# Kernel optimization log

Hardware: AMD Instinct MI355X
Metric: run time of the kernel (lower is better)

The kernel has to match this reference:

```python
import jax, jax.numpy as jnp
import numpy as np

NUM_GRAPHS = 128

def setup_inputs() -> dict:
    key = jax.random.key(0)
    ks = jax.random.split(key, 12)
    N, E = 50000, 800000
    x = jax.random.normal(ks[0], (N, 54), dtype=jnp.float32)
    edge_index = jax.random.randint(ks[1], (2, E), 0, N, dtype=jnp.int64)
    batch = jnp.sort(jax.random.randint(ks[2], (N,), 0, NUM_GRAPHS, dtype=jnp.int64))
    def lin(k, fi, fo):
        return jax.random.normal(k, (fi, fo), dtype=jnp.float32) / np.sqrt(fi)
    return {
        "x": x, "edge_index": edge_index, "batch": batch,
        "W1l": lin(ks[3], 54, 128), "b1": jnp.zeros((128,), jnp.float32), "W1r": lin(ks[4], 54, 128),
        "W2l": lin(ks[5], 128, 256), "b2": jnp.zeros((256,), jnp.float32), "W2r": lin(ks[6], 128, 256),
        "W3l": lin(ks[7], 256, 256), "b3": jnp.zeros((256,), jnp.float32), "W3r": lin(ks[8], 256, 256),
    }

def _sage(h, src, dst, n, Wl, b, Wr):
    # sum-aggregate neighbor features x_j (j=src) into node i (i=dst), then
    # out = lin_l(agg) + lin_r(h)  (PyG SAGEConv, aggr='sum')
    agg = jax.ops.segment_sum(h[src], dst, num_segments=n)
    return jax.nn.relu(agg @ Wl + b + h @ Wr)

def reference(x, edge_index, batch, W1l, b1, W1r, W2l, b2, W2r, W3l, b3, W3r):
    n = x.shape[0]
    src, dst = edge_index[0], edge_index[1]
    h = _sage(x, src, dst, n, W1l, b1, W1r)
    h = _sage(h, src, dst, n, W2l, b2, W2r)
    h = _sage(h, src, dst, n, W3l, b3, W3r)
    # global mean pool per graph (gep = global_mean_pool)
    sums = jax.ops.segment_sum(h, batch, num_segments=NUM_GRAPHS)
    cnts = jax.ops.segment_sum(jnp.ones((n, 1), h.dtype), batch, num_segments=NUM_GRAPHS)
    return sums / jnp.maximum(cnts, 1.0)
```

## Files before the change

### kernel.cpp

```cpp
#include <hip/hip_runtime.h>


typedef unsigned short u16;
typedef __attribute__((ext_vector_type(8))) short bf16x8;
typedef __attribute__((ext_vector_type(4))) float f32x4;

__device__ __forceinline__ u16 f2b(float f) {
    union { float f; unsigned u; } v; v.f = f;
    unsigned u = v.u;
    return (u16)((u + 0x7FFF + ((u >> 16) & 1)) >> 16);
}
__device__ __forceinline__ float b2f(u16 h) {
    union { unsigned u; float f; } v; v.u = ((unsigned)h) << 16;
    return v.f;
}
__device__ __forceinline__ float blo(unsigned u) {
    union { unsigned u; float f; } v; v.u = u << 16;
    return v.f;
}
__device__ __forceinline__ float bhi(unsigned u) {
    union { unsigned u; float f; } v; v.u = u & 0xffff0000u;
    return v.f;
}

__global__ void k_prep(const float* __restrict__ x,
                       const float* __restrict__ W1l, const float* __restrict__ W1r,
                       const float* __restrict__ W2l, const float* __restrict__ W2r,
                       const float* __restrict__ W3l, const float* __restrict__ W3r,
                       u16* __restrict__ xb,
                       u16* __restrict__ wt1l, u16* __restrict__ wt1r,
                       u16* __restrict__ wt2l, u16* __restrict__ wt2r,
                       u16* __restrict__ wt3l, u16* __restrict__ wt3r, int N) {
    long idx = (long)blockIdx.x * 256 + threadIdx.x;
    long s0 = (long)N * 54;
    if (idx < s0) { xb[idx] = f2b(x[idx]); return; }
    idx -= s0;
    if (idx < 2 * 128 * 64) {
        u16* o = (idx < 128 * 64) ? wt1l : wt1r;
        const float* w = (idx < 128 * 64) ? W1l : W1r;
        long loc = idx % (128 * 64);
        int d = (int)(loc >> 6), k = (int)(loc & 63);
        o[loc] = (k < 54) ? f2b(w[(long)k * 128 + d]) : 0;
        return;
    }
    idx -= 2 * 128 * 64;
    if (idx < 2 * 256 * 128) {
        u16* o = (idx < 256 * 128) ? wt2l : wt2r;
        const float* w = (idx < 256 * 128) ? W2l : W2r;
        long loc = idx % (256 * 128);
        int d = (int)(loc >> 7), k = (int)(loc & 127);
        o[loc] = f2b(w[(long)k * 256 + d]);
        return;
    }
    idx -= 2 * 256 * 128;
    if (idx < 2 * 256 * 256) {
        u16* o = (idx < 256 * 256) ? wt3l : wt3r;
        const float* w = (idx < 256 * 256) ? W3l : W3r;
        long loc = idx % (256 * 256);
        int d = (int)(loc >> 8), k = (int)(loc & 255);
        o[loc] = f2b(w[(long)k * 256 + d]);
    }
}

__global__ void k_count(const int* __restrict__ dst, int* __restrict__ cnt, int E) {
    int e = blockIdx.x * 256 + threadIdx.x;
    if (e < E) atomicAdd(&cnt[dst[e]], 1);
}

__global__ void k_bsum(const int* __restrict__ cnt, int* __restrict__ bsum, int N) {
    __shared__ int sm[256];
    int i = blockIdx.x * 256 + threadIdx.x;
    sm[threadIdx.x] = (i < N) ? cnt[i] : 0;
    __syncthreads();
    for (int off = 128; off > 0; off >>= 1) {
        if (threadIdx.x < off) sm[threadIdx.x] += sm[threadIdx.x + off];
        __syncthreads();
    }
    if (threadIdx.x == 0) bsum[blockIdx.x] = sm[0];
}

__global__ void k_bscan(const int* __restrict__ bsum, int* __restrict__ boff, int NB) {
    __shared__ int sm[256];
    int t = threadIdx.x;
    int v = (t < NB) ? bsum[t] : 0;
    sm[t] = v;
    __syncthreads();
    for (int off = 1; off < 256; off <<= 1) {
        int add = (t >= off) ? sm[t - off] : 0;
        __syncthreads();
        sm[t] += add;
        __syncthreads();
    }
    if (t < NB) boff[t] = sm[t] - v;
}

__global__ void k_scan(const int* __restrict__ cnt, const int* __restrict__ boff,
                       int* __restrict__ rowptr, int* __restrict__ wpos, int N, int E) {
    __shared__ int sm[256];
    int t = threadIdx.x;
    int i = blockIdx.x * 256 + t;
    int v = (i < N) ? cnt[i] : 0;
    sm[t] = v;
    __syncthreads();
    for (int off = 1; off < 256; off <<= 1) {
        int add = (t >= off) ? sm[t - off] : 0;
        __syncthreads();
        sm[t] += add;
        __syncthreads();
    }
    int ex = sm[t] - v + boff[blockIdx.x];
    if (i < N) { rowptr[i] = ex; wpos[i] = ex; }
    if (i == 0) rowptr[N] = E;
}

__global__ void k_fill(const int* __restrict__ src, const int* __restrict__ dst,
                       int* __restrict__ wpos, int* __restrict__ csr, int E) {
    int e = blockIdx.x * 256 + threadIdx.x;
    if (e < E) {
        int p = atomicAdd(&wpos[dst[e]], 1);
        csr[p] = src[e];
    }
}

template <int KA, int KW, int DOUT, int EPW>
__global__ __launch_bounds__(512) void k_fused(const u16* __restrict__ h,
                                               const int* __restrict__ rowptr,
                                               const int* __restrict__ csr,
                                               const u16* __restrict__ Wt1,
                                               const u16* __restrict__ Wt2,
                                               const float* __restrict__ bias,
                                               u16* __restrict__ C, int N) {
    constexpr int KAP = KW + 8;
    constexpr int WCOL = DOUT / 4;
    constexpr int FN = WCOL / 16;
    __shared__ u16 aggL[64 * KAP];
    __shared__ u16 xL[(KA == 54) ? 64 * KAP : 8];
    __shared__ u16 Bs[DOUT * 40];

    const int tid = threadIdx.x;
    const int w = tid >> 6, lane = tid & 63;
    const int m0 = blockIdx.x * 64;

    for (int t = 0; t < 8; ++t) {
        int r = w * 8 + t;
        int node = m0 + r;
        if constexpr (KA == 54) {
            u16 xv = 0;
            if (node < N && lane < 54) xv = h[(size_t)node * 54 + lane];
            xL[r * KAP + lane] = xv;
            float a = 0.f;
            if (node < N && lane < 54) {
                int b0 = rowptr[node], b1 = rowptr[node + 1];
                #pragma unroll 8
                for (int b = b0; b < b1; ++b)
                    a += b2f(h[(size_t)csr[b] * 54 + lane]);
            }
            aggL[r * KAP + lane] = f2b(a);
        } else {
            constexpr int GRP = 64 / EPW;
            static_assert(KA == GRP * 8, "geometry");
            int sub = lane / GRP, dl = lane % GRP;
            float a0 = 0.f, a1 = 0.f, a2 = 0.f, a3 = 0.f;
            float a4 = 0.f, a5 = 0.f, a6 = 0.f, a7 = 0.f;
            if (node < N) {
                int b0 = rowptr[node], b1 = rowptr[node + 1];
                int b = b0;
                #pragma unroll 4
                for (; b + EPW <= b1; b += EPW) {
                    int s = csr[b + sub];
                    uint4 v = *reinterpret_cast<const uint4*>(h + (size_t)s * KA + dl * 8);
                    a0 += blo(v.x); a1 += bhi(v.x);
                    a2 += blo(v.y); a3 += bhi(v.y);
                    a4 += blo(v.z); a5 += bhi(v.z);
                    a6 += blo(v.w); a7 += bhi(v.w);
                }
                int rem = b1 - b;
                if (sub < rem) {
                    int s = csr[b + sub];
                    uint4 v = *reinterpret_cast<const uint4*>(h + (size_t)s * KA + dl * 8);
                    a0 += blo(v.x); a1 += bhi(v.x);
                    a2 += blo(v.y); a3 += bhi(v.y);
                    a4 += blo(v.z); a5 += bhi(v.z);
                    a6 += blo(v.w); a7 += bhi(v.w);
                }
            }
            #pragma unroll
            for (int off = GRP; off < 64; off <<= 1) {
                a0 += __shfl_xor(a0, off, 64);
                a1 += __shfl_xor(a1, off, 64);
                a2 += __shfl_xor(a2, off, 64);
                a3 += __shfl_xor(a3, off, 64);
                a4 += __shfl_xor(a4, off, 64);
                a5 += __shfl_xor(a5, off, 64);
                a6 += __shfl_xor(a6, off, 64);
                a7 += __shfl_xor(a7, off, 64);
            }
            if (sub == 0) {
                uint4 o;
                o.x = ((unsigned)f2b(a0)) | (((unsigned)f2b(a1)) << 16);
                o.y = ((unsigned)f2b(a2)) | (((unsigned)f2b(a3)) << 16);
                o.z = ((unsigned)f2b(a4)) | (((unsigned)f2b(a5)) << 16);
                o.w = ((unsigned)f2b(a6)) | (((unsigned)f2b(a7)) << 16);
                *reinterpret_cast<uint4*>(&aggL[r * KAP + dl * 8]) = o;
            }
        }
    }
    __syncthreads();

    const int wr = w >> 2, wc = w & 3;
    const int lo = lane & 15, hi = lane >> 4;

    f32x4 acc[2][FN];
    #pragma unroll
    for (int i = 0; i < 2; ++i)
        #pragma unroll
        for (int j = 0; j < FN; ++j) acc[i][j] = {0.f, 0.f, 0.f, 0.f};

    constexpr int KT = KW / 32;

    #pragma unroll
    for (int s = 0; s < 2; ++s) {
        const u16* __restrict__ Wp = s ? Wt2 : Wt1;
        for (int kt = 0; kt < KT; ++kt) {
            const int k0 = kt * 32;
            #pragma unroll
            for (int it = 0; it < DOUT / 128; ++it) {
                int v = it * 512 + tid;
                int r = v >> 2, c = v & 3;
                uint4 val = *reinterpret_cast<const uint4*>(Wp + (size_t)r * KW + k0 + c * 8);
                *reinterpret_cast<uint4*>(&Bs[r * 40 + c * 8]) = val;
            }
            __syncthreads();
            bf16x8 bfr[2];
            if (s == 0) {
                #pragma unroll
                for (int fm = 0; fm < 2; ++fm)
                    bfr[fm] = *reinterpret_cast<const bf16x8*>(&aggL[(wr * 32 + fm * 16 + lo) * KAP + k0 + hi * 8]);
            } else if constexpr (KA == 54) {
                #pragma unroll
                for (int fm = 0; fm < 2; ++fm)
                    bfr[fm] = *reinterpret_cast<const bf16x8*>(&xL[(wr * 32 + fm * 16 + lo) * KAP + k0 + hi * 8]);
            } else {
                #pragma unroll
                for (int fm = 0; fm < 2; ++fm) {
                    int m = m0 + wr * 32 + fm * 16 + lo;
                    bf16x8 z = {0, 0, 0, 0, 0, 0, 0, 0};
                    bfr[fm] = (m < N) ? *reinterpret_cast<const bf16x8*>(h + (size_t)m * KA + k0 + hi * 8) : z;
                }
            }
            #pragma unroll
            for (int fn = 0; fn < FN; ++fn) {
                bf16x8 af = *reinterpret_cast<const bf16x8*>(&Bs[(wc * WCOL + fn * 16 + lo) * 40 + hi * 8]);
                #pragma unroll
                for (int fm = 0; fm < 2; ++fm)
                    acc[fm][fn] = __builtin_amdgcn_mfma_f32_16x16x32_bf16(af, bfr[fm], acc[fm][fn], 0, 0, 0);
            }
            __syncthreads();
        }
    }
    #pragma unroll
    for (int fm = 0; fm < 2; ++fm) {
        int node = m0 + wr * 32 + fm * 16 + lo;
        if (node < N) {
            #pragma unroll
            for (int fn = 0; fn < FN; ++fn) {
                int fb = wc * WCOL + fn * 16 + hi * 4;
                float4 bv = *reinterpret_cast<const float4*>(bias + fb);
                ushort4 o;
                o.x = f2b(fmaxf(acc[fm][fn][0] + bv.x, 0.f));
                o.y = f2b(fmaxf(acc[fm][fn][1] + bv.y, 0.f));
                o.z = f2b(fmaxf(acc[fm][fn][2] + bv.z, 0.f));
                o.w = f2b(fmaxf(acc[fm][fn][3] + bv.w, 0.f));
                *reinterpret_cast<ushort4*>(C + (size_t)node * DOUT + fb) = o;
            }
        }
    }
}

template <int ROWS>
__global__ void k_pool(const u16* __restrict__ h3, const int* __restrict__ batch,
                       float* __restrict__ outsum, int* __restrict__ cnt, int N) {
    int r0 = blockIdx.x * ROWS;
    int r1 = min(r0 + ROWS, N);
    if (r0 >= N) return;
    int d = threadIdx.x;
    int cur = batch[r0];
    float s = 0.f;
    int c = 0;
    for (int i = r0; i < r1; ++i) {
        int g = batch[i];
        if (g != cur) {
            atomicAdd(&outsum[cur * 256 + d], s);
            if (d == 0) atomicAdd(&cnt[cur], c);
            s = 0.f; c = 0; cur = g;
        }
        s += b2f(h3[(size_t)i * 256 + d]);
        c++;
    }
    atomicAdd(&outsum[cur * 256 + d], s);
    if (d == 0) atomicAdd(&cnt[cur], c);
}

__global__ void k_div(float* __restrict__ out, const int* __restrict__ cnt, int total) {
    int idx = blockIdx.x * 256 + threadIdx.x;
    if (idx < total) {
        float c = fmaxf((float)cnt[idx >> 8], 1.0f);
        out[idx] = out[idx] / c;
    }
}

extern "C" void kernel_launch(void* const* d_in, const int* in_sizes, int n_in,
                              void* d_out, int out_size, void* d_ws, size_t ws_size,
                              hipStream_t stream) {
    const float* x   = (const float*)d_in[0];
    const int* ei    = (const int*)d_in[1];
    const int* batch = (const int*)d_in[2];
    const float* W1l = (const float*)d_in[3];
    const float* b1  = (const float*)d_in[4];
    const float* W1r = (const float*)d_in[5];
    const float* W2l = (const float*)d_in[6];
    const float* b2  = (const float*)d_in[7];
    const float* W2r = (const float*)d_in[8];
    const float* W3l = (const float*)d_in[9];
    const float* b3  = (const float*)d_in[10];
    const float* W3r = (const float*)d_in[11];

    const int N = in_sizes[0] / 54;
    const int E = in_sizes[1] / 2;
    const int* src = ei;
    const int* dst = ei + E;

    u16* xb   = (u16*)d_ws;
    u16* buf1 = xb + (size_t)N * 54;
    u16* buf2 = buf1 + (size_t)N * 256;
    u16* wt1l = buf2 + (size_t)N * 256;
    u16* wt1r = wt1l + 128 * 64;
    u16* wt2l = wt1r + 128 * 64;
    u16* wt2r = wt2l + 256 * 128;
    u16* wt3l = wt2r + 256 * 128;
    u16* wt3r = wt3l + 256 * 256;
    int* ip = (int*)(wt3r + 256 * 256);
    int* cntdeg  = ip; ip += N;
    int* rowptr  = ip; ip += N + 1;
    int* wpos    = ip; ip += N + 1;
    int* bsum    = ip; ip += 256;
    int* boff    = ip; ip += 256;
    int* cntpool = ip; ip += 128;
    int* csr     = ip;

    hipMemsetAsync(cntdeg, 0, (size_t)N * sizeof(int), stream);
    hipMemsetAsync(d_out, 0, (size_t)out_size * sizeof(float), stream);
    hipMemsetAsync(cntpool, 0, 128 * sizeof(int), stream);

    const int NB = (N + 255) / 256;
    const int EB = (E + 255) / 256;

    {
        long total = (long)N * 54 + 2L * 128 * 64 + 2L * 256 * 128 + 2L * 256 * 256;
        int g = (int)((total + 255) / 256);
        k_prep<<<g, 256, 0, stream>>>(x, W1l, W1r, W2l, W2r, W3l, W3r,
                                      xb, wt1l, wt1r, wt2l, wt2r, wt3l, wt3r, N);
    }

    k_count<<<EB, 256, 0, stream>>>(dst, cntdeg, E);
    k_bsum<<<NB, 256, 0, stream>>>(cntdeg, bsum, N);
    k_bscan<<<1, 256, 0, stream>>>(bsum, boff, NB);
    k_scan<<<NB, 256, 0, stream>>>(cntdeg, boff, rowptr, wpos, N, E);
    k_fill<<<EB, 256, 0, stream>>>(src, dst, wpos, csr, E);

    const int GB = (N + 63) / 64;

    k_fused<54, 64, 128, 1><<<GB, 512, 0, stream>>>(xb, rowptr, csr, wt1l, wt1r, b1, buf1, N);
    k_fused<128, 128, 256, 4><<<GB, 512, 0, stream>>>(buf1, rowptr, csr, wt2l, wt2r, b2, buf2, N);
    k_fused<256, 256, 256, 2><<<GB, 512, 0, stream>>>(buf2, rowptr, csr, wt3l, wt3r, b3, buf1, N);

    k_pool<32><<<(N + 31) / 32, 256, 0, stream>>>(buf1, batch, (float*)d_out, cntpool, N);
    k_div<<<(out_size + 255) / 256, 256, 0, stream>>>((float*)d_out, cntpool, out_size);
}
```

Before: 365.0 us.

## Split SAGE layers into concurrent gather/root-GEMM kernel plus neighbor GEMM

Each layer's fused gather+GEMM kernel is replaced by two kernels. The first runs, in one grid, blocks that compute the root term h@Wr into the output buffer alongside blocks that gather neighbor sums into a scratch buffer with one wave per node. The second computes agg@Wl and adds bias, the stored root term and ReLU. The aim is to overlap gather-bound and MFMA-bound work and to give the gather more parallelism. It also pads x to 64 columns and folds degree counting into the prep kernel, at the cost of extra global round trips for the aggregate and root intermediates.

New measurement: 341.0 us. 1.07x faster.

```diff
diff --git a/kernel.cpp b/kernel.cpp
--- a/kernel.cpp
+++ b/kernel.cpp
@@ -27,13 +27,19 @@
                        const float* __restrict__ W1l, const float* __restrict__ W1r,
                        const float* __restrict__ W2l, const float* __restrict__ W2r,
                        const float* __restrict__ W3l, const float* __restrict__ W3r,
+                       const int* __restrict__ dst, int* __restrict__ cntdeg,
                        u16* __restrict__ xb,
                        u16* __restrict__ wt1l, u16* __restrict__ wt1r,
                        u16* __restrict__ wt2l, u16* __restrict__ wt2r,
-                       u16* __restrict__ wt3l, u16* __restrict__ wt3r, int N) {
+                       u16* __restrict__ wt3l, u16* __restrict__ wt3r,
+                       int N, int E) {
     long idx = (long)blockIdx.x * 256 + threadIdx.x;
-    long s0 = (long)N * 54;
-    if (idx < s0) { xb[idx] = f2b(x[idx]); return; }
+    long s0 = (long)N * 64;
+    if (idx < s0) {
+        int row = (int)(idx >> 6), k = (int)(idx & 63);
+        xb[idx] = (k < 54) ? f2b(x[(size_t)row * 54 + k]) : 0;
+        return;
+    }
     idx -= s0;
     if (idx < 2 * 128 * 64) {
         u16* o = (idx < 128 * 64) ? wt1l : wt1r;
@@ -59,12 +65,10 @@
         long loc = idx % (256 * 256);
         int d = (int)(loc >> 8), k = (int)(loc & 255);
         o[loc] = f2b(w[(long)k * 256 + d]);
-    }
-}
-
-__global__ void k_count(const int* __restrict__ dst, int* __restrict__ cnt, int E) {
-    int e = blockIdx.x * 256 + threadIdx.x;
-    if (e < E) atomicAdd(&cnt[dst[e]], 1);
+        return;
+    }
+    idx -= 2 * 256 * 256;
+    if (idx < E) atomicAdd(&cntdeg[dst[idx]], 1);
 }
 
 __global__ void k_bsum(const int* __restrict__ cnt, int* __restrict__ bsum, int N) {
@@ -122,141 +126,188 @@
     }
 }
 
-template <int KA, int KW, int DOUT, int EPW>
-__global__ __launch_bounds__(512) void k_fused(const u16* __restrict__ h,
-                                               const int* __restrict__ rowptr,
-                                               const int* __restrict__ csr,
-                                               const u16* __restrict__ Wt1,
-                                               const u16* __restrict__ Wt2,
-                                               const float* __restrict__ bias,
-                                               u16* __restrict__ C, int N) {
-    constexpr int KAP = KW + 8;
+template <int KA, int DOUT, int EPW>
+__global__ __launch_bounds__(512) void k_comb(const u16* __restrict__ h,
+                                              const int* __restrict__ rowptr,
+                                              const int* __restrict__ csr,
+                                              const u16* __restrict__ Wtr,
+                                              u16* __restrict__ bufA,
+                                              u16* __restrict__ yR,
+                                              int GR, int N) {
+    constexpr int BKP = 40;
     constexpr int WCOL = DOUT / 4;
     constexpr int FN = WCOL / 16;
-    __shared__ u16 aggL[64 * KAP];
-    __shared__ u16 xL[(KA == 54) ? 64 * KAP : 8];
-    __shared__ u16 Bs[DOUT * 40];
-
-    const int tid = threadIdx.x;
-    const int w = tid >> 6, lane = tid & 63;
-    const int m0 = blockIdx.x * 64;
-
-    for (int t = 0; t < 8; ++t) {
-        int r = w * 8 + t;
-        int node = m0 + r;
-        if constexpr (KA == 54) {
-            u16 xv = 0;
-            if (node < N && lane < 54) xv = h[(size_t)node * 54 + lane];
-            xL[r * KAP + lane] = xv;
-            float a = 0.f;
-            if (node < N && lane < 54) {
-                int b0 = rowptr[node], b1 = rowptr[node + 1];
-                #pragma unroll 8
-                for (int b = b0; b < b1; ++b)
-                    a += b2f(h[(size_t)csr[b] * 54 + lane]);
-            }
-            aggL[r * KAP + lane] = f2b(a);
-        } else {
-            constexpr int GRP = 64 / EPW;
-            static_assert(KA == GRP * 8, "geometry");
-            int sub = lane / GRP, dl = lane % GRP;
-            float a0 = 0.f, a1 = 0.f, a2 = 0.f, a3 = 0.f;
-            float a4 = 0.f, a5 = 0.f, a6 = 0.f, a7 = 0.f;
-            if (node < N) {
-                int b0 = rowptr[node], b1 = rowptr[node + 1];
-                int b = b0;
-                #pragma unroll 4
-                for (; b + EPW <= b1; b += EPW) {
-                    int s = csr[b + sub];
-                    uint4 v = *reinterpret_cast<const uint4*>(h + (size_t)s * KA + dl * 8);
-                    a0 += blo(v.x); a1 += bhi(v.x);
-                    a2 += blo(v.y); a3 += bhi(v.y);
-                    a4 += blo(v.z); a5 += bhi(v.z);
-                    a6 += blo(v.w); a7 += bhi(v.w);
-                }
-                int rem = b1 - b;
-                if (sub < rem) {
-                    int s = csr[b + sub];
-                    uint4 v = *reinterpret_cast<const uint4*>(h + (size_t)s * KA + dl * 8);
-                    a0 += blo(v.x); a1 += bhi(v.x);
-                    a2 += blo(v.y); a3 += bhi(v.y);
-                    a4 += blo(v.z); a5 += bhi(v.z);
-                    a6 += blo(v.w); a7 += bhi(v.w);
-                }
-            }
-            #pragma unroll
-            for (int off = GRP; off < 64; off <<= 1) {
-                a0 += __shfl_xor(a0, off, 64);
-                a1 += __shfl_xor(a1, off, 64);
-                a2 += __shfl_xor(a2, off, 64);
-                a3 += __shfl_xor(a3, off, 64);
-                a4 += __shfl_xor(a4, off, 64);
-                a5 += __shfl_xor(a5, off, 64);
-                a6 += __shfl_xor(a6, off, 64);
-                a7 += __shfl_xor(a7, off, 64);
-            }
-            if (sub == 0) {
-                uint4 o;
-                o.x = ((unsigned)f2b(a0)) | (((unsigned)f2b(a1)) << 16);
-                o.y = ((unsigned)f2b(a2)) | (((unsigned)f2b(a3)) << 16);
-                o.z = ((unsigned)f2b(a4)) | (((unsigned)f2b(a5)) << 16);
-                o.w = ((unsigned)f2b(a6)) | (((unsigned)f2b(a7)) << 16);
-                *reinterpret_cast<uint4*>(&aggL[r * KAP + dl * 8]) = o;
-            }
-        }
-    }
-    __syncthreads();
-
-    const int wr = w >> 2, wc = w & 3;
-    const int lo = lane & 15, hi = lane >> 4;
-
-    f32x4 acc[2][FN];
-    #pragma unroll
-    for (int i = 0; i < 2; ++i)
-        #pragma unroll
-        for (int j = 0; j < FN; ++j) acc[i][j] = {0.f, 0.f, 0.f, 0.f};
-
-    constexpr int KT = KW / 32;
-
-    #pragma unroll
-    for (int s = 0; s < 2; ++s) {
-        const u16* __restrict__ Wp = s ? Wt2 : Wt1;
+    __shared__ u16 As[64 * BKP];
+    __shared__ u16 Bs[DOUT * BKP];
+
+    if ((int)blockIdx.x < GR) {
+        const int tid = threadIdx.x;
+        const int w = tid >> 6, lane = tid & 63;
+        const int wr = w >> 2, wc = w & 3;
+        const int lo = lane & 15, hi = lane >> 4;
+        const int m0 = blockIdx.x * 64;
+
+        f32x4 acc[2][FN];
+        #pragma unroll
+        for (int i = 0; i < 2; ++i)
+            #pragma unroll
+            for (int j = 0; j < FN; ++j) acc[i][j] = {0.f, 0.f, 0.f, 0.f};
+
+        constexpr int KT = KA / 32;
         for (int kt = 0; kt < KT; ++kt) {
             const int k0 = kt * 32;
             #pragma unroll
             for (int it = 0; it < DOUT / 128; ++it) {
                 int v = it * 512 + tid;
                 int r = v >> 2, c = v & 3;
-                uint4 val = *reinterpret_cast<const uint4*>(Wp + (size_t)r * KW + k0 + c * 8);
-                *reinterpret_cast<uint4*>(&Bs[r * 40 + c * 8]) = val;
+                uint4 val = *reinterpret_cast<const uint4*>(Wtr + (size_t)r * KA + k0 + c * 8);
+                *reinterpret_cast<uint4*>(&Bs[r * BKP + c * 8]) = val;
+            }
+            if (tid < 256) {
+                int r = tid >> 2, c = tid & 3;
+                int m = m0 + r;
+                uint4 val = {0u, 0u, 0u, 0u};
+                if (m < N) val = *reinterpret_cast<const uint4*>(h + (size_t)m * KA + k0 + c * 8);
+                *reinterpret_cast<uint4*>(&As[r * BKP + c * 8]) = val;
             }
             __syncthreads();
             bf16x8 bfr[2];
-            if (s == 0) {
-                #pragma unroll
-                for (int fm = 0; fm < 2; ++fm)
-                    bfr[fm] = *reinterpret_cast<const bf16x8*>(&aggL[(wr * 32 + fm * 16 + lo) * KAP + k0 + hi * 8]);
-            } else if constexpr (KA == 54) {
-                #pragma unroll
-                for (int fm = 0; fm < 2; ++fm)
-                    bfr[fm] = *reinterpret_cast<const bf16x8*>(&xL[(wr * 32 + fm * 16 + lo) * KAP + k0 + hi * 8]);
-            } else {
-                #pragma unroll
-                for (int fm = 0; fm < 2; ++fm) {
-                    int m = m0 + wr * 32 + fm * 16 + lo;
-                    bf16x8 z = {0, 0, 0, 0, 0, 0, 0, 0};
-                    bfr[fm] = (m < N) ? *reinterpret_cast<const bf16x8*>(h + (size_t)m * KA + k0 + hi * 8) : z;
-                }
-            }
+            #pragma unroll
+            for (int fm = 0; fm < 2; ++fm)
+                bfr[fm] = *reinterpret_cast<const bf16x8*>(&As[(wr * 32 + fm * 16 + lo) * BKP + hi * 8]);
             #pragma unroll
             for (int fn = 0; fn < FN; ++fn) {
-                bf16x8 af = *reinterpret_cast<const bf16x8*>(&Bs[(wc * WCOL + fn * 16 + lo) * 40 + hi * 8]);
+                bf16x8 af = *reinterpret_cast<const bf16x8*>(&Bs[(wc * WCOL + fn * 16 + lo) * BKP + hi * 8]);
                 #pragma unroll
                 for (int fm = 0; fm < 2; ++fm)
                     acc[fm][fn] = __builtin_amdgcn_mfma_f32_16x16x32_bf16(af, bfr[fm], acc[fm][fn], 0, 0, 0);
             }
             __syncthreads();
         }
+        #pragma unroll
+        for (int fm = 0; fm < 2; ++fm) {
+            int node = m0 + wr * 32 + fm * 16 + lo;
+            if (node < N) {
+                #pragma unroll
+                for (int fn = 0; fn < FN; ++fn) {
+                    int fb = wc * WCOL + fn * 16 + hi * 4;
+                    ushort4 o;
+                    o.x = f2b(acc[fm][fn][0]);
+                    o.y = f2b(acc[fm][fn][1]);
+                    o.z = f2b(acc[fm][fn][2]);
+                    o.w = f2b(acc[fm][fn][3]);
+                    *reinterpret_cast<ushort4*>(yR + (size_t)node * DOUT + fb) = o;
+                }
+            }
+        }
+    } else {
+        constexpr int GRP = 64 / EPW;
+        static_assert(KA == GRP * 8, "geometry");
+        const int gb = (int)blockIdx.x - GR;
+        const int w = threadIdx.x >> 6, lane = threadIdx.x & 63;
+        const int i = gb * 8 + w;
+        if (i >= N) return;
+        int b0 = rowptr[i], b1 = rowptr[i + 1];
+        int sub = lane / GRP;
+        int dl = lane % GRP;
+
+        float a0 = 0.f, a1 = 0.f, a2 = 0.f, a3 = 0.f;
+        float a4 = 0.f, a5 = 0.f, a6 = 0.f, a7 = 0.f;
+
+        int b = b0;
+        #pragma unroll 4
+        for (; b + EPW <= b1; b += EPW) {
+            int s = csr[b + sub];
+            uint4 v = *reinterpret_cast<const uint4*>(h + (size_t)s * KA + dl * 8);
+            a0 += blo(v.x); a1 += bhi(v.x);
+            a2 += blo(v.y); a3 += bhi(v.y);
+            a4 += blo(v.z); a5 += bhi(v.z);
+            a6 += blo(v.w); a7 += bhi(v.w);
+        }
+        int rem = b1 - b;
+        if (sub < rem) {
+            int s = csr[b + sub];
+            uint4 v = *reinterpret_cast<const uint4*>(h + (size_t)s * KA + dl * 8);
+            a0 += blo(v.x); a1 += bhi(v.x);
+            a2 += blo(v.y); a3 += bhi(v.y);
+            a4 += blo(v.z); a5 += bhi(v.z);
+            a6 += blo(v.w); a7 += bhi(v.w);
+        }
+        #pragma unroll
+        for (int off = GRP; off < 64; off <<= 1) {
+            a0 += __shfl_xor(a0, off, 64);
+            a1 += __shfl_xor(a1, off, 64);
+            a2 += __shfl_xor(a2, off, 64);
+            a3 += __shfl_xor(a3, off, 64);
+            a4 += __shfl_xor(a4, off, 64);
+            a5 += __shfl_xor(a5, off, 64);
+            a6 += __shfl_xor(a6, off, 64);
+            a7 += __shfl_xor(a7, off, 64);
+        }
+        if (sub == 0) {
+            uint4 o;
+            o.x = ((unsigned)f2b(a0)) | (((unsigned)f2b(a1)) << 16);
+            o.y = ((unsigned)f2b(a2)) | (((unsigned)f2b(a3)) << 16);
+            o.z = ((unsigned)f2b(a4)) | (((unsigned)f2b(a5)) << 16);
+            o.w = ((unsigned)f2b(a6)) | (((unsigned)f2b(a7)) << 16);
+            *reinterpret_cast<uint4*>(bufA + (size_t)i * KA + dl * 8) = o;
+        }
+    }
+}
+
+template <int KA, int DOUT>
+__global__ __launch_bounds__(512) void k_gemmL(const u16* __restrict__ A,
+                                               const u16* __restrict__ Wtl,
+                                               const float* __restrict__ bias,
+                                               u16* __restrict__ C, int N) {
+    constexpr int BKP = 40;
+    constexpr int WCOL = DOUT / 4;
+    constexpr int FN = WCOL / 16;
+    __shared__ u16 As[64 * BKP];
+    __shared__ u16 Bs[DOUT * BKP];
+
+    const int tid = threadIdx.x;
+    const int w = tid >> 6, lane = tid & 63;
+    const int wr = w >> 2, wc = w & 3;
+    const int lo = lane & 15, hi = lane >> 4;
+    const int m0 = blockIdx.x * 64;
+
+    f32x4 acc[2][FN];
+    #pragma unroll
+    for (int i = 0; i < 2; ++i)
+        #pragma unroll
+        for (int j = 0; j < FN; ++j) acc[i][j] = {0.f, 0.f, 0.f, 0.f};
+
+    constexpr int KT = KA / 32;
+    for (int kt = 0; kt < KT; ++kt) {
+        const int k0 = kt * 32;
+        #pragma unroll
+        for (int it = 0; it < DOUT / 128; ++it) {
+            int v = it * 512 + tid;
+            int r = v >> 2, c = v & 3;
+            uint4 val = *reinterpret_cast<const uint4*>(Wtl + (size_t)r * KA + k0 + c * 8);
+            *reinterpret_cast<uint4*>(&Bs[r * BKP + c * 8]) = val;
+        }
+        if (tid < 256) {
+            int r = tid >> 2, c = tid & 3;
+            int m = m0 + r;
+            uint4 val = {0u, 0u, 0u, 0u};
+            if (m < N) val = *reinterpret_cast<const uint4*>(A + (size_t)m * KA + k0 + c * 8);
+            *reinterpret_cast<uint4*>(&As[r * BKP + c * 8]) = val;
+        }
+        __syncthreads();
+        bf16x8 bfr[2];
+        #pragma unroll
+        for (int fm = 0; fm < 2; ++fm)
+            bfr[fm] = *reinterpret_cast<const bf16x8*>(&As[(wr * 32 + fm * 16 + lo) * BKP + hi * 8]);
+        #pragma unroll
+        for (int fn = 0; fn < FN; ++fn) {
+            bf16x8 af = *reinterpret_cast<const bf16x8*>(&Bs[(wc * WCOL + fn * 16 + lo) * BKP + hi * 8]);
+            #pragma unroll
+            for (int fm = 0; fm < 2; ++fm)
+                acc[fm][fn] = __builtin_amdgcn_mfma_f32_16x16x32_bf16(af, bfr[fm], acc[fm][fn], 0, 0, 0);
+        }
+        __syncthreads();
     }
     #pragma unroll
     for (int fm = 0; fm < 2; ++fm) {
@@ -266,11 +317,12 @@
             for (int fn = 0; fn < FN; ++fn) {
                 int fb = wc * WCOL + fn * 16 + hi * 4;
                 float4 bv = *reinterpret_cast<const float4*>(bias + fb);
+                ushort4 yv = *reinterpret_cast<const ushort4*>(C + (size_t)node * DOUT + fb);
                 ushort4 o;
-                o.x = f2b(fmaxf(acc[fm][fn][0] + bv.x, 0.f));
-                o.y = f2b(fmaxf(acc[fm][fn][1] + bv.y, 0.f));
-                o.z = f2b(fmaxf(acc[fm][fn][2] + bv.z, 0.f));
-                o.w = f2b(fmaxf(acc[fm][fn][3] + bv.w, 0.f));
+                o.x = f2b(fmaxf(acc[fm][fn][0] + bv.x + b2f(yv.x), 0.f));
+                o.y = f2b(fmaxf(acc[fm][fn][1] + bv.y + b2f(yv.y), 0.f));
+                o.z = f2b(fmaxf(acc[fm][fn][2] + bv.z + b2f(yv.z), 0.f));
+                o.w = f2b(fmaxf(acc[fm][fn][3] + bv.w + b2f(yv.w), 0.f));
                 *reinterpret_cast<ushort4*>(C + (size_t)node * DOUT + fb) = o;
             }
         }
@@ -331,7 +383,8 @@
     const int* dst = ei + E;
 
     u16* xb   = (u16*)d_ws;
-    u16* buf1 = xb + (size_t)N * 54;
+    u16* bufA = xb + (size_t)N * 64;
+    u16* buf1 = bufA + (size_t)N * 256;
     u16* buf2 = buf1 + (size_t)N * 256;
     u16* wt1l = buf2 + (size_t)N * 256;
     u16* wt1r = wt1l + 128 * 64;
@@ -356,23 +409,27 @@
     const int EB = (E + 255) / 256;
 
     {
-        long total = (long)N * 54 + 2L * 128 * 64 + 2L * 256 * 128 + 2L * 256 * 256;
+        long total = (long)N * 64 + 2L * 128 * 64 + 2L * 256 * 128 + 2L * 256 * 256 + E;
         int g = (int)((total + 255) / 256);
         k_prep<<<g, 256, 0, stream>>>(x, W1l, W1r, W2l, W2r, W3l, W3r,
-                                      xb, wt1l, wt1r, wt2l, wt2r, wt3l, wt3r, N);
-    }
-
-    k_count<<<EB, 256, 0, stream>>>(dst, cntdeg, E);
+                                      dst, cntdeg,
+                                      xb, wt1l, wt1r, wt2l, wt2r, wt3l, wt3r, N, E);
+    }
+
     k_bsum<<<NB, 256, 0, stream>>>(cntdeg, bsum, N);
     k_bscan<<<1, 256, 0, stream>>>(bsum, boff, NB);
     k_scan<<<NB, 256, 0, stream>>>(cntdeg, boff, rowptr, wpos, N, E);
     k_fill<<<EB, 256, 0, stream>>>(src, dst, wpos, csr, E);
 
-    const int GB = (N + 63) / 64;
-
-    k_fused<54, 64, 128, 1><<<GB, 512, 0, stream>>>(xb, rowptr, csr, wt1l, wt1r, b1, buf1, N);
-    k_fused<128, 128, 256, 4><<<GB, 512, 0, stream>>>(buf1, rowptr, csr, wt2l, wt2r, b2, buf2, N);
-    k_fused<256, 256, 256, 2><<<GB, 512, 0, stream>>>(buf2, rowptr, csr, wt3l, wt3r, b3, buf1, N);
+    const int GR = (N + 63) / 64;
+    const int GGB = (N + 7) / 8;
+
+    k_comb<64, 128, 8><<<GR + GGB, 512, 0, stream>>>(xb, rowptr, csr, wt1r, bufA, buf1, GR, N);
+    k_gemmL<64, 128><<<GR, 512, 0, stream>>>(bufA, wt1l, b1, buf1, N);
+    k_comb<128, 256, 4><<<GR + GGB, 512, 0, stream>>>(buf1, rowptr, csr, wt2r, bufA, buf2, GR, N);
+    k_gemmL<128, 256><<<GR, 512, 0, stream>>>(bufA, wt2l, b2, buf2, N);
+    k_comb<256, 256, 2><<<GR + GGB, 512, 0, stream>>>(buf2, rowptr, csr, wt3r, bufA, buf1, GR, N);
+    k_gemmL<256, 256><<<GR, 512, 0, stream>>>(bufA, wt3l, b3, buf1, N);
 
     k_pool<32><<<(N + 31) / 32, 256, 0, stream>>>(buf1, batch, (float*)d_out, cntpool, N);
     k_div<<<(out_size + 255) / 256, 256, 0, stream>>>((float*)d_out, cntpool, out_size);
```
